# Kernel optimization log

Hardware: AMD Instinct MI355X
Metric: run time of the kernel (lower is better)

Reference implementation:

```python
import jax, jax.numpy as jnp
import numpy as np

B, T, D = 32, 256, 384
MAX_LEN = 2048

def setup_inputs() -> dict:
    key = jax.random.key(0)
    k1, k2 = jax.random.split(key)
    x = jax.random.normal(k1, (B, T, D), dtype=jnp.float32)
    duration = jax.random.randint(k2, (B, T), 0, 16, dtype=jnp.int32)
    return {"x": x, "duration": duration, "max_len": MAX_LEN}

def reference(x, duration, max_len):
    # x: [B, T, D]; duration: [B, T] int; max_len: python int
    # Each input vector x[b, i] is repeated duration[b, i] times along the time
    # axis; results are concatenated and padded/truncated to max_len with zeros.
    csum = jnp.cumsum(duration, axis=1)                     # [B, T] inclusive cumsum
    total = csum[:, -1]                                      # [B] true expanded lengths
    mel_len = jnp.minimum(total, max_len)                    # [B]
    pos = jnp.arange(max_len, dtype=csum.dtype)              # [L]
    # Output frame j comes from source index = first i with csum[i] > j
    idx = jax.vmap(lambda c: jnp.searchsorted(c, pos, side='right'))(csum)  # [B, L]
    idx = jnp.clip(idx, 0, x.shape[1] - 1)
    out = jnp.take_along_axis(x, idx[:, :, None], axis=1)    # [B, L, D]
    valid = pos[None, :] < mel_len[:, None]                  # [B, L]
    out = jnp.where(valid[..., None], out, jnp.zeros((), dtype=x.dtype))
    return out, mel_len.astype(jnp.int32)
```

## Files before the change

kernel.cpp:

```cpp
#include <hip/hip_runtime.h>

#define B_  32
#define T_  256
#define D_  384
#define ML_ 2048
#define ROWS_PER_BLK 32
#define CHUNKS (ML_ / ROWS_PER_BLK)

__global__ __launch_bounds__(256) void lr_fused_kernel(
    const float4* __restrict__ x4,
    const int*    __restrict__ dur,
    const int*    __restrict__ max_len_p,
    float4*       __restrict__ out4,
    float*        __restrict__ mel_out)
{
    const int blk   = blockIdx.x;
    const int b     = blk >> 6;
    const int chunk = blk & (CHUNKS - 1);
    const int tid   = threadIdx.x;

    __shared__ int cs[T_];
    __shared__ int ridx[ROWS_PER_BLK];

    cs[tid] = dur[b * T_ + tid];
    __syncthreads();

    #pragma unroll
    for (int off = 1; off < T_; off <<= 1) {
        int v = (tid >= off) ? cs[tid - off] : 0;
        __syncthreads();
        cs[tid] += v;
        __syncthreads();
    }

    const int total = cs[T_ - 1];
    const int mel   = min(total, max_len_p[0]);
    if (chunk == 0 && tid == 0) mel_out[b] = (float)mel;

    if (tid < ROWS_PER_BLK) {
        const int pos = chunk * ROWS_PER_BLK + tid;
        int r = -1;
        if (pos < mel) {
            int lo = 0, hi = T_;
            #pragma unroll
            for (int s = 0; s < 8; ++s) {
                int mid = (lo + hi) >> 1;
                if (cs[mid] <= pos) lo = mid + 1; else hi = mid;
            }
            r = min(lo, T_ - 1);
        }
        ridx[tid] = r;
    }
    __syncthreads();

    const int rowsz = D_ / 4;
    const float4* xb = x4 + (size_t)b * T_ * rowsz;
    float4* ob = out4 + ((size_t)b * ML_ + (size_t)chunk * ROWS_PER_BLK) * rowsz;
    const int N = ROWS_PER_BLK * rowsz;

    #pragma unroll 4
    for (int i = tid; i < N; i += 256) {
        const int rl   = i / rowsz;
        const int lane = i - rl * rowsz;
        const int idx  = ridx[rl];
        float4 v = (idx >= 0) ? xb[idx * rowsz + lane]
                              : make_float4(0.f, 0.f, 0.f, 0.f);
        ob[i] = v;
    }
}

extern "C" void kernel_launch(void* const* d_in, const int* in_sizes, int n_in,
                              void* d_out, int out_size, void* d_ws, size_t ws_size,
                              hipStream_t stream) {
    const float* x       = (const float*)d_in[0];
    const int*   dur     = (const int*)d_in[1];
    const int*   max_len = (const int*)d_in[2];
    float*       out     = (float*)d_out;
    float*       mel_out = out + (size_t)B_ * ML_ * D_;

    lr_fused_kernel<<<B_ * CHUNKS, 256, 0, stream>>>(
        (const float4*)x, dur, max_len, (float4*)out, mel_out);
}
```

Measured before the change: 24.79 us.

## Use wavefront shuffle scan, larger row chunks, and nontemporal output stores

Replaces the shared-memory Hillis-Steele prefix sum, which needs many block barriers, with a 64-lane shuffle scan plus a small cross-wave offset pass. Doubles rows per block so each block's scan cost is spread over more output rows, which halves the block count. Output writes become nontemporal stores so the large write-only stream bypasses cache retention. Fewer blocks may reduce occupancy and latency hiding on a memory-bound copy.

Result: slower. 25.29 us (+2.0%).

```diff
diff --git a/kernel.cpp b/kernel.cpp
--- a/kernel.cpp
+++ b/kernel.cpp
@@ -4,34 +4,42 @@
 #define T_  256
 #define D_  384
 #define ML_ 2048
-#define ROWS_PER_BLK 32
+#define ROWS_PER_BLK 64
 #define CHUNKS (ML_ / ROWS_PER_BLK)
 
+typedef float f4 __attribute__((ext_vector_type(4)));
+
 __global__ __launch_bounds__(256) void lr_fused_kernel(
-    const float4* __restrict__ x4,
-    const int*    __restrict__ dur,
-    const int*    __restrict__ max_len_p,
-    float4*       __restrict__ out4,
-    float*        __restrict__ mel_out)
+    const f4* __restrict__ x4,
+    const int* __restrict__ dur,
+    const int* __restrict__ max_len_p,
+    f4*        __restrict__ out4,
+    float*     __restrict__ mel_out)
 {
     const int blk   = blockIdx.x;
-    const int b     = blk >> 6;
+    const int b     = blk >> 5;
     const int chunk = blk & (CHUNKS - 1);
     const int tid   = threadIdx.x;
+    const int lane  = tid & 63;
+    const int wid   = tid >> 6;
 
     __shared__ int cs[T_];
+    __shared__ int wtot[4];
     __shared__ int ridx[ROWS_PER_BLK];
 
-    cs[tid] = dur[b * T_ + tid];
+    int v = dur[b * T_ + tid];
+    #pragma unroll
+    for (int d = 1; d < 64; d <<= 1) {
+        int n = __shfl_up(v, d);
+        if (lane >= d) v += n;
+    }
+    if (lane == 63) wtot[wid] = v;
     __syncthreads();
-
+    int off = 0;
     #pragma unroll
-    for (int off = 1; off < T_; off <<= 1) {
-        int v = (tid >= off) ? cs[tid - off] : 0;
-        __syncthreads();
-        cs[tid] += v;
-        __syncthreads();
-    }
+    for (int w = 0; w < 3; ++w) if (w < wid) off += wtot[w];
+    cs[tid] = v + off;
+    __syncthreads();
 
     const int total = cs[T_ - 1];
     const int mel   = min(total, max_len_p[0]);
@@ -54,18 +62,19 @@
     __syncthreads();
 
     const int rowsz = D_ / 4;
-    const float4* xb = x4 + (size_t)b * T_ * rowsz;
-    float4* ob = out4 + ((size_t)b * ML_ + (size_t)chunk * ROWS_PER_BLK) * rowsz;
+    const f4* xb = x4 + (size_t)b * T_ * rowsz;
+    f4* ob = out4 + ((size_t)b * ML_ + (size_t)chunk * ROWS_PER_BLK) * rowsz;
     const int N = ROWS_PER_BLK * rowsz;
 
     #pragma unroll 4
     for (int i = tid; i < N; i += 256) {
         const int rl   = i / rowsz;
-        const int lane = i - rl * rowsz;
+        const int ln   = i - rl * rowsz;
         const int idx  = ridx[rl];
-        float4 v = (idx >= 0) ? xb[idx * rowsz + lane]
-                              : make_float4(0.f, 0.f, 0.f, 0.f);
-        ob[i] = v;
+        f4 w;
+        if (idx >= 0) w = xb[idx * rowsz + ln];
+        else          w = (f4){0.f, 0.f, 0.f, 0.f};
+        __builtin_nontemporal_store(w, &ob[i]);
     }
 }
 
@@ -79,5 +88,5 @@
     float*       mel_out = out + (size_t)B_ * ML_ * D_;
 
     lr_fused_kernel<<<B_ * CHUNKS, 256, 0, stream>>>(
-        (const float4*)x, dur, max_len, (float4*)out, mel_out);
+        (const f4*)x, dur, max_len, (f4*)out, mel_out);
 }
```
